# Performance work log

Measured on AMD Instinct MI355X. Metric: run time of the kernel, lower is better.

The kernel has to match this reference:

```python
import jax, jax.numpy as jnp
import numpy as np

B, F, E, H, D = 8192, 50, 64, 2, 8  # batch, fields, embed, heads, domains
HD = E // H
EPS = 1e-6


def setup_inputs() -> dict:
    key = jax.random.key(0)
    ks = jax.random.split(key, 8)
    std = 0.05  # matches nn.init.normal_(std=0.05) over ALL params (incl. layernorm)
    inputs = jax.random.normal(ks[0], (B, F, E), jnp.float32)
    domain_ids = jax.random.randint(ks[1], (B,), 1, D + 1)  # values 1..D as in torch masks
    W_Query_domains = jax.random.normal(ks[2], (D, E, E), jnp.float32) * std
    W_key = jax.random.normal(ks[3], (E, E), jnp.float32) * std
    W_Value = jax.random.normal(ks[4], (E, E), jnp.float32) * std
    W_Res = jax.random.normal(ks[5], (E, E), jnp.float32) * std
    ln_scale = jax.random.normal(ks[6], (D, E), jnp.float32) * std
    ln_bias = jax.random.normal(ks[7], (D, E), jnp.float32) * std
    return dict(inputs=inputs, domain_ids=domain_ids, W_Query_domains=W_Query_domains,
                W_key=W_key, W_Value=W_Value, W_Res=W_Res,
                ln_scale=ln_scale, ln_bias=ln_bias)


def reference(inputs, domain_ids, W_Query_domains, W_key, W_Value, W_Res, ln_scale, ln_bias):
    # Eval mode: dropouts are identity. merge='no' so shared W_Query is unused.
    b, f, e = inputs.shape
    idx = domain_ids - 1  # 0-based domain index per row

    # Shared keys/values projections
    keys = jnp.einsum('bfe,eo->bfo', inputs, W_key)
    values = jnp.einsum('bfe,eo->bfo', inputs, W_Value)

    # Per-row query weight gather (replaces the python loop over domains)
    Wq = W_Query_domains[idx]  # [B,E,E]
    querys = jnp.einsum('bfe,beo->bfo', inputs, Wq)

    # Split heads: contiguous chunks of size HD along embed dim -> [B,F,H,HD]
    q = querys.reshape(b, f, H, HD)
    k = keys.reshape(b, f, H, HD)
    v = values.reshape(b, f, H, HD)

    scores = jnp.einsum('bihd,bjhd->bhij', q, k) / np.sqrt(HD).astype(np.float32)
    attn = jax.nn.softmax(scores, axis=-1)
    out = jnp.einsum('bhij,bjhd->bihd', attn, v).reshape(b, f, e)  # head concat order matches torch

    out = out + jnp.einsum('bfe,eo->bfo', inputs, W_Res)  # residual via W_Res
    out = jax.nn.relu(out)

    # Per-domain LayerNorm (gather gamma/beta per row)
    gamma = ln_scale[idx][:, None, :]  # [B,1,E]
    beta = ln_bias[idx][:, None, :]
    mean = jnp.mean(out, axis=-1, keepdims=True)
    var = jnp.mean(jnp.square(out - mean), axis=-1, keepdims=True)
    out = (out - mean) * jax.lax.rsqrt(var + EPS) * gamma + beta
    return out
```

## Files before the change

kernel.cpp:

```cpp
#include <hip/hip_runtime.h>
#include <hip/hip_bf16.h>

#define NB    8192
#define NF    50
#define NE    64

typedef __attribute__((ext_vector_type(8))) short short8;
typedef __attribute__((ext_vector_type(4))) short short4v;
typedef __attribute__((ext_vector_type(4))) float float4v;

static constexpr float SM_C   = 0.25509667991878083f;
static constexpr float LN_EPS = 1e-6f;

#define MFMA(a, b, c) __builtin_amdgcn_mfma_f32_16x16x32_bf16((a), (b), (c), 0, 0, 0)

__device__ __forceinline__ unsigned short f2bf(float f) {
    return __bfloat16_as_ushort(__float2bfloat16(f));
}

__device__ __forceinline__ int soff(int row, int col) {
    return row * 64 + ((((col >> 3) ^ row) & 7) << 3) + (col & 7);
}

__device__ __forceinline__ void st_pack4(unsigned short* p, float4v v) {
    union { unsigned short u[4]; short4v s; } r;
    r.u[0] = f2bf(v.x); r.u[1] = f2bf(v.y); r.u[2] = f2bf(v.z); r.u[3] = f2bf(v.w);
    *(short4v*)p = r.s;
}

__device__ __forceinline__ float fexp2(float x) {
#if __has_builtin(__builtin_amdgcn_exp2f)
    return __builtin_amdgcn_exp2f(x);
#else
    float r; asm("v_exp_f32 %0, %1" : "=v"(r) : "v"(x)); return r;
#endif
}

__device__ __forceinline__ float frcp(float x) {
#if __has_builtin(__builtin_amdgcn_rcpf)
    return __builtin_amdgcn_rcpf(x);
#else
    return 1.f / x;
#endif
}

__global__ void prep_weights(const float* __restrict__ wq, const float* __restrict__ wk,
                             const float* __restrict__ wv, const float* __restrict__ wr,
                             unsigned short* __restrict__ ws) {
    int i = blockIdx.x * 256 + threadIdx.x;
    if (i >= 11 * 4096) return;
    int m = i >> 12, t = i & 4095, o = t >> 6, e = t & 63;
    float v;
    if (m < 8) {
        int po = (o & 32) | ((o & 12) << 1) | (((o >> 4) & 1) << 2) | (o & 3);
        v = wq[(m * 64 + e) * 64 + po];
    }
    else if (m == 8) v = wk[e * 64 + o] * SM_C;
    else if (m == 9) v = wv[e * 64 + o];
    else             v = wr[e * 64 + o];
    ws[i] = f2bf(v);
}

__global__ __launch_bounds__(256, 3)
void mdr_mfma(const float* __restrict__ x_g, const int* __restrict__ dom_g,
              const unsigned short* __restrict__ ws,
              const float* __restrict__ gam_g, const float* __restrict__ bet_g,
              float* __restrict__ out_g) {
    __shared__ __align__(16) unsigned short L[6 * NE * NE];

    const int tid = threadIdx.x;
    const int lm  = tid & 15;
    const int lg  = (tid >> 4) & 3;
    const int w   = tid >> 6;
    const int b0  = blockIdx.x * 2;

    int dom[2];
    dom[0] = dom_g[b0] - 1;
    dom[1] = dom_g[b0 + 1] - 1;

    unsigned short* xs[2] = {L,            L + 3 * 4096};
    unsigned short* Kb[2] = {L + 1 * 4096, L + 4 * 4096};
    unsigned short* Vt[2] = {L + 2 * 4096, L + 5 * 4096};

    {
        #pragma unroll
        for (int it = 0; it < 8; ++it) {
            int s  = tid + it * 256;
            int rr = s >> 10;
            int t  = s & 1023;
            int r  = t >> 4, c4 = t & 15;
            const float* xb = x_g + (size_t)(b0 + rr) * (NF * NE);
            float4v v = {0.f, 0.f, 0.f, 0.f};
            if (r < NF) v = *(const float4v*)(xb + t * 4);
            st_pack4(L + rr * 3 * 4096 + soff(r, c4 * 4), v);
        }
    }

    short8 vw0, vw1, kw[4][2];
    {
        const unsigned short* wv = ws + 9 * 4096;
        vw0 = *(const short8*)(wv + (lm + 16 * w) * 64 + 8 * lg);
        vw1 = *(const short8*)(wv + (lm + 16 * w) * 64 + 8 * lg + 32);
        const unsigned short* wk = ws + 8 * 4096;
        #pragma unroll
        for (int mt = 0; mt < 4; ++mt) {
            kw[mt][0] = *(const short8*)(wk + (lm + 16 * mt) * 64 + 8 * lg);
            kw[mt][1] = *(const short8*)(wk + (lm + 16 * mt) * 64 + 8 * lg + 32);
        }
    }
    __syncthreads();

    #pragma unroll
    for (int mt = 0; mt < 4; ++mt) {
        #pragma unroll
        for (int rr = 0; rr < 2; ++rr) {
            short8 xv0 = *(const short8*)(xs[rr] + soff(lm + 16 * mt, 8 * lg));
            short8 xv1 = *(const short8*)(xs[rr] + soff(lm + 16 * mt, 8 * lg + 32));
            float4v acc = {0.f, 0.f, 0.f, 0.f};
            acc = MFMA(xv0, vw0, acc);
            acc = MFMA(xv1, vw1, acc);
            st_pack4(Vt[rr] + soff(lm + 16 * w, 32 * (mt >> 1) + 8 * lg + 4 * (mt & 1)), acc);
        }
    }

    short8 xfw[2][2];
    #pragma unroll
    for (int rr = 0; rr < 2; ++rr) {
        xfw[rr][0] = *(const short8*)(xs[rr] + soff(lm + 16 * w, 8 * lg));
        xfw[rr][1] = *(const short8*)(xs[rr] + soff(lm + 16 * w, 8 * lg + 32));
    }

    #pragma unroll
    for (int mt = 0; mt < 4; ++mt) {
        #pragma unroll
        for (int rr = 0; rr < 2; ++rr) {
            float4v acc = {0.f, 0.f, 0.f, 0.f};
            acc = MFMA(kw[mt][0], xfw[rr][0], acc);
            acc = MFMA(kw[mt][1], xfw[rr][1], acc);
            st_pack4(Kb[rr] + soff(lm + 16 * w, 16 * mt + 4 * lg), acc);
        }
    }

    short8 qfrag[2][2];
    #pragma unroll
    for (int rr = 0; rr < 2; ++rr) {
        const unsigned short* wq = ws + dom[rr] * 4096;
        #pragma unroll
        for (int h = 0; h < 2; ++h) {
            float4v a0, a1;
            {
                short8 qw0 = *(const short8*)(wq + (lm + 16 * (2 * h)) * 64 + 8 * lg);
                short8 qw1 = *(const short8*)(wq + (lm + 16 * (2 * h)) * 64 + 8 * lg + 32);
                float4v z = {0.f, 0.f, 0.f, 0.f};
                z = MFMA(qw0, xfw[rr][0], z);
                a0 = MFMA(qw1, xfw[rr][1], z);
            }
            {
                short8 qw0 = *(const short8*)(wq + (lm + 16 * (2 * h + 1)) * 64 + 8 * lg);
                short8 qw1 = *(const short8*)(wq + (lm + 16 * (2 * h + 1)) * 64 + 8 * lg + 32);
                float4v z = {0.f, 0.f, 0.f, 0.f};
                z = MFMA(qw0, xfw[rr][0], z);
                a1 = MFMA(qw1, xfw[rr][1], z);
            }
            union { unsigned short u[8]; short8 s; } r;
            #pragma unroll
            for (int r4 = 0; r4 < 4; ++r4) {
                r.u[r4]     = f2bf(a0[r4]);
                r.u[4 + r4] = f2bf(a1[r4]);
            }
            qfrag[rr][h] = r.s;
        }
    }
    __syncthreads();

    short8 rw[4][2];
    {
        const unsigned short* wr = ws + 10 * 4096;
        #pragma unroll
        for (int nt = 0; nt < 4; ++nt) {
            rw[nt][0] = *(const short8*)(wr + (lm + 16 * nt) * 64 + 8 * lg);
            rw[nt][1] = *(const short8*)(wr + (lm + 16 * nt) * 64 + 8 * lg + 32);
        }
    }

    short8 pa[2][2][2];
    #pragma unroll
    for (int rr = 0; rr < 2; ++rr) {
        #pragma unroll
        for (int h = 0; h < 2; ++h) {
            float p[4][4];
            float sum = 0.f;
            #pragma unroll
            for (int mt = 0; mt < 4; ++mt) {
                short8 kf = *(const short8*)(Kb[rr] + soff(lm + 16 * mt, 32 * h + 8 * lg));
                float4v z = {0.f, 0.f, 0.f, 0.f};
                float4v s = MFMA(kf, qfrag[rr][h], z);
                #pragma unroll
                for (int r = 0; r < 4; ++r) {
                    float e = fexp2(s[r]);
                    p[mt][r] = e; sum += e;
                }
            }
            sum += __shfl_xor(sum, 16);
            sum += __shfl_xor(sum, 32);
            sum -= 14.f;
            const float ri = frcp(sum);
            #pragma unroll
            for (int ks = 0; ks < 2; ++ks) {
                union { unsigned short u[8]; short8 s; } r;
                #pragma unroll
                for (int r4 = 0; r4 < 4; ++r4) {
                    r.u[r4]     = f2bf(p[2 * ks][r4] * ri);
                    r.u[4 + r4] = f2bf(p[2 * ks + 1][r4] * ri);
                }
                pa[rr][h][ks] = r.s;
            }
        }
    }

    float4v oacc[2][4];
    #pragma unroll
    for (int rr = 0; rr < 2; ++rr)
        #pragma unroll
        for (int c = 0; c < 4; ++c) {
            oacc[rr][c].x = 0.f; oacc[rr][c].y = 0.f;
            oacc[rr][c].z = 0.f; oacc[rr][c].w = 0.f;
        }
    #pragma unroll
    for (int h = 0; h < 2; ++h)
        #pragma unroll
        for (int nt2 = 0; nt2 < 2; ++nt2) {
            const int c = 2 * h + nt2;
            #pragma unroll
            for (int rr = 0; rr < 2; ++rr) {
                short8 vf0 = *(const short8*)(Vt[rr] + soff(16 * c + lm, 8 * lg));
                short8 vf1 = *(const short8*)(Vt[rr] + soff(16 * c + lm, 8 * lg + 32));
                oacc[rr][c] = MFMA(pa[rr][h][0], vf0, oacc[rr][c]);
                oacc[rr][c] = MFMA(pa[rr][h][1], vf1, oacc[rr][c]);
            }
        }

    #pragma unroll
    for (int nt = 0; nt < 4; ++nt) {
        #pragma unroll
        for (int rr = 0; rr < 2; ++rr) {
            oacc[rr][nt] = MFMA(xfw[rr][0], rw[nt][0], oacc[rr][nt]);
            oacc[rr][nt] = MFMA(xfw[rr][1], rw[nt][1], oacc[rr][nt]);
        }
    }

    #pragma unroll
    for (int rr = 0; rr < 2; ++rr) {
        float gm[4], bt[4];
        #pragma unroll
        for (int c = 0; c < 4; ++c) {
            gm[c] = gam_g[dom[rr] * 64 + 16 * c + lm];
            bt[c] = bet_g[dom[rr] * 64 + 16 * c + lm];
        }
        float v[4][4], s1[4], s2[4];
        #pragma unroll
        for (int r = 0; r < 4; ++r) {
            #pragma unroll
            for (int c = 0; c < 4; ++c) v[r][c] = fmaxf(oacc[rr][c][r], 0.f);
            s1[r] = v[r][0] + v[r][1] + v[r][2] + v[r][3];
            s2[r] = v[r][0]*v[r][0] + v[r][1]*v[r][1] + v[r][2]*v[r][2] + v[r][3]*v[r][3];
        }
        #pragma unroll
        for (int msk = 1; msk < 16; msk <<= 1) {
            #pragma unroll
            for (int r = 0; r < 4; ++r) {
                s1[r] += __shfl_xor(s1[r], msk);
                s2[r] += __shfl_xor(s2[r], msk);
            }
        }
        #pragma unroll
        for (int r = 0; r < 4; ++r) {
            const float mean = s1[r] * (1.f / 64.f);
            const float var  = s2[r] * (1.f / 64.f) - mean * mean;
            const float rs   = rsqrtf(var + LN_EPS);
            const int f = 4 * lg + r + 16 * w;
            if (f < NF) {
                float* op = out_g + (size_t)(b0 + rr) * (NF * NE) + f * 64 + lm;
                #pragma unroll
                for (int c = 0; c < 4; ++c)
                    op[16 * c] = (v[r][c] - mean) * rs * gm[c] + bt[c];
            }
        }
    }
}

extern "C" void kernel_launch(void* const* d_in, const int* in_sizes, int n_in,
                              void* d_out, int out_size, void* d_ws, size_t ws_size,
                              hipStream_t stream) {
    const float* x   = (const float*)d_in[0];
    const int*   dom = (const int*)  d_in[1];
    const float* wq  = (const float*)d_in[2];
    const float* wk  = (const float*)d_in[3];
    const float* wv  = (const float*)d_in[4];
    const float* wr  = (const float*)d_in[5];
    const float* gam = (const float*)d_in[6];
    const float* bet = (const float*)d_in[7];
    unsigned short* ws = (unsigned short*)d_ws;
    float* out = (float*)d_out;

    hipLaunchKernelGGL(prep_weights, dim3(176), dim3(256), 0, stream, wq, wk, wv, wr, ws);
    hipLaunchKernelGGL(mdr_mfma, dim3(NB / 2), dim3(256), 0, stream,
                       x, dom, ws, gam, bet, out);
}
```

Before: 102.2 us.

## Alias V-transpose buffer onto x tile in LDS to raise occupancy

Shared memory per block drops from six 4096-element tiles to four. The transposed V tile now reuses the x staging buffer: V results are held in registers (vacc) until after the barrier that ends x use, then written to LDS, with an extra __syncthreads added. The launch-bounds occupancy hint rises from 3 to 5 blocks per CU to exploit the smaller LDS footprint. The cost is more live registers across the Q/K phase and one more barrier, which could cause register spills under the tighter bound.

```diff
diff --git a/kernel.cpp b/kernel.cpp
--- a/kernel.cpp
+++ b/kernel.cpp
@@ -13,6 +13,9 @@
 static constexpr float LN_EPS = 1e-6f;
 
 #define MFMA(a, b, c) __builtin_amdgcn_mfma_f32_16x16x32_bf16((a), (b), (c), 0, 0, 0)
+
+#define XSVT(rr) (L + (rr) * 4096)
+#define KBB(rr)  (L + 8192 + (rr) * 4096)
 
 __device__ __forceinline__ unsigned short f2bf(float f) {
     return __bfloat16_as_ushort(__float2bfloat16(f));
@@ -61,12 +64,12 @@
     ws[i] = f2bf(v);
 }
 
-__global__ __launch_bounds__(256, 3)
+__global__ __launch_bounds__(256, 5)
 void mdr_mfma(const float* __restrict__ x_g, const int* __restrict__ dom_g,
               const unsigned short* __restrict__ ws,
               const float* __restrict__ gam_g, const float* __restrict__ bet_g,
               float* __restrict__ out_g) {
-    __shared__ __align__(16) unsigned short L[6 * NE * NE];
+    __shared__ __align__(16) unsigned short L[4 * NE * NE];
 
     const int tid = threadIdx.x;
     const int lm  = tid & 15;
@@ -77,10 +80,6 @@
     int dom[2];
     dom[0] = dom_g[b0] - 1;
     dom[1] = dom_g[b0 + 1] - 1;
-
-    unsigned short* xs[2] = {L,            L + 3 * 4096};
-    unsigned short* Kb[2] = {L + 1 * 4096, L + 4 * 4096};
-    unsigned short* Vt[2] = {L + 2 * 4096, L + 5 * 4096};
 
     {
         #pragma unroll
@@ -92,7 +91,7 @@
             const float* xb = x_g + (size_t)(b0 + rr) * (NF * NE);
             float4v v = {0.f, 0.f, 0.f, 0.f};
             if (r < NF) v = *(const float4v*)(xb + t * 4);
-            st_pack4(L + rr * 3 * 4096 + soff(r, c4 * 4), v);
+            st_pack4(XSVT(rr) + soff(r, c4 * 4), v);
         }
     }
 
@@ -110,24 +109,11 @@
     }
     __syncthreads();
 
-    #pragma unroll
-    for (int mt = 0; mt < 4; ++mt) {
-        #pragma unroll
-        for (int rr = 0; rr < 2; ++rr) {
-            short8 xv0 = *(const short8*)(xs[rr] + soff(lm + 16 * mt, 8 * lg));
-            short8 xv1 = *(const short8*)(xs[rr] + soff(lm + 16 * mt, 8 * lg + 32));
-            float4v acc = {0.f, 0.f, 0.f, 0.f};
-            acc = MFMA(xv0, vw0, acc);
-            acc = MFMA(xv1, vw1, acc);
-            st_pack4(Vt[rr] + soff(lm + 16 * w, 32 * (mt >> 1) + 8 * lg + 4 * (mt & 1)), acc);
-        }
-    }
-
     short8 xfw[2][2];
     #pragma unroll
     for (int rr = 0; rr < 2; ++rr) {
-        xfw[rr][0] = *(const short8*)(xs[rr] + soff(lm + 16 * w, 8 * lg));
-        xfw[rr][1] = *(const short8*)(xs[rr] + soff(lm + 16 * w, 8 * lg + 32));
+        xfw[rr][0] = *(const short8*)(XSVT(rr) + soff(lm + 16 * w, 8 * lg));
+        xfw[rr][1] = *(const short8*)(XSVT(rr) + soff(lm + 16 * w, 8 * lg + 32));
     }
 
     #pragma unroll
@@ -137,7 +123,20 @@
             float4v acc = {0.f, 0.f, 0.f, 0.f};
             acc = MFMA(kw[mt][0], xfw[rr][0], acc);
             acc = MFMA(kw[mt][1], xfw[rr][1], acc);
-            st_pack4(Kb[rr] + soff(lm + 16 * w, 16 * mt + 4 * lg), acc);
+            st_pack4(KBB(rr) + soff(lm + 16 * w, 16 * mt + 4 * lg), acc);
+        }
+    }
+
+    float4v vacc[2][4];
+    #pragma unroll
+    for (int mt = 0; mt < 4; ++mt) {
+        #pragma unroll
+        for (int rr = 0; rr < 2; ++rr) {
+            short8 xv0 = *(const short8*)(XSVT(rr) + soff(lm + 16 * mt, 8 * lg));
+            short8 xv1 = *(const short8*)(XSVT(rr) + soff(lm + 16 * mt, 8 * lg + 32));
+            float4v acc = {0.f, 0.f, 0.f, 0.f};
+            acc = MFMA(xv0, vw0, acc);
+            vacc[rr][mt] = MFMA(xv1, vw1, acc);
         }
     }
 
@@ -173,6 +172,14 @@
     }
     __syncthreads();
 
+    #pragma unroll
+    for (int mt = 0; mt < 4; ++mt)
+        #pragma unroll
+        for (int rr = 0; rr < 2; ++rr)
+            st_pack4(XSVT(rr) + soff(lm + 16 * w, 32 * (mt >> 1) + 8 * lg + 4 * (mt & 1)),
+                     vacc[rr][mt]);
+    __syncthreads();
+
     short8 rw[4][2];
     {
         const unsigned short* wr = ws + 10 * 4096;
@@ -192,7 +199,7 @@
             float sum = 0.f;
             #pragma unroll
             for (int mt = 0; mt < 4; ++mt) {
-                short8 kf = *(const short8*)(Kb[rr] + soff(lm + 16 * mt, 32 * h + 8 * lg));
+                short8 kf = *(const short8*)(KBB(rr) + soff(lm + 16 * mt, 32 * h + 8 * lg));
                 float4v z = {0.f, 0.f, 0.f, 0.f};
                 float4v s = MFMA(kf, qfrag[rr][h], z);
                 #pragma unroll
@@ -233,8 +240,8 @@
             const int c = 2 * h + nt2;
             #pragma unroll
             for (int rr = 0; rr < 2; ++rr) {
-                short8 vf0 = *(const short8*)(Vt[rr] + soff(16 * c + lm, 8 * lg));
-                short8 vf1 = *(const short8*)(Vt[rr] + soff(16 * c + lm, 8 * lg + 32));
+                short8 vf0 = *(const short8*)(XSVT(rr) + soff(16 * c + lm, 8 * lg));
+                short8 vf1 = *(const short8*)(XSVT(rr) + soff(16 * c + lm, 8 * lg + 32));
                 oacc[rr][c] = MFMA(pa[rr][h][0], vf0, oacc[rr][c]);
                 oacc[rr][c] = MFMA(pa[rr][h][1], vf1, oacc[rr][c]);
             }
```

Result: faster. 95.25 us (-6.8%).
